# Performance work log

Hardware: AMD Instinct MI355X
Metric: run time of the kernel (lower is better)

## Reference

```python
import jax, jax.numpy as jnp
import numpy as np

D = 64        # GatedGraphConv out_channels
N_LAYERS = 5  # number of stacked convs


def setup_inputs() -> dict:
    key = jax.random.key(0)
    ks = jax.random.split(key, 16)
    N, E, G = 100000, 1600000, 64
    s = 0.1
    inp = {
        'conv_weight': jax.random.normal(ks[0], (N_LAYERS, D, D), jnp.float32) * s,
        'gru_w_ih':    jax.random.normal(ks[1], (N_LAYERS, 3 * D, D), jnp.float32) * s,
        'gru_w_hh':    jax.random.normal(ks[2], (N_LAYERS, 3 * D, D), jnp.float32) * s,
        'gru_b_ih':    jax.random.normal(ks[3], (N_LAYERS, 3 * D), jnp.float32) * s,
        'gru_b_hh':    jax.random.normal(ks[4], (N_LAYERS, 3 * D), jnp.float32) * s,
        'fc1_w': jax.random.normal(ks[5], (32, D), jnp.float32) * s,
        'fc1_b': jax.random.normal(ks[6], (32,), jnp.float32) * s,
        'fc2_w': jax.random.normal(ks[7], (16, 32), jnp.float32) * s,
        'fc2_b': jax.random.normal(ks[8], (16,), jnp.float32) * s,
        'fc3_w': jax.random.normal(ks[9], (1, 16), jnp.float32) * s,
        'fc3_b': jax.random.normal(ks[10], (1,), jnp.float32) * s,
        'edge_index': jax.random.randint(ks[11], (2, E), 0, N, jnp.int64 if jax.config.jax_enable_x64 else jnp.int32),
        'batch': jnp.sort(jax.random.randint(ks[12], (N,), 0, G, jnp.int32)),
        'num_nodes': N,
        'num_graphs': G,
    }
    return inp


def _gru_cell(m, h, w_ih, w_hh, b_ih, b_hh):
    # torch.nn.GRUCell math; m: [N,D] input, h: [N,D] hidden
    gi = m @ w_ih.T + b_ih   # [N, 3D]
    gh = h @ w_hh.T + b_hh   # [N, 3D]
    i_r, i_z, i_n = jnp.split(gi, 3, axis=1)
    h_r, h_z, h_n = jnp.split(gh, 3, axis=1)
    r = jax.nn.sigmoid(i_r + h_r)
    z = jax.nn.sigmoid(i_z + h_z)
    n = jnp.tanh(i_n + r * h_n)
    return (1.0 - z) * n + z * h


def reference(conv_weight, gru_w_ih, gru_w_hh, gru_b_ih, gru_b_hh,
              fc1_w, fc1_b, fc2_w, fc2_b, fc3_w, fc3_b,
              edge_index, batch, num_nodes, num_graphs):
    src, dst = edge_index[0], edge_index[1]  # source_to_target flow
    # initial node features: zeros [N,8] zero-padded to D by GatedGraphConv
    x0 = jnp.zeros((num_nodes, D), jnp.float32)

    def step(x, params):
        w, wih, whh, bih, bhh = params
        m = x @ w                                        # [N, D]
        agg = jax.ops.segment_sum(m[src], dst, num_segments=num_nodes)  # scatter-add
        return _gru_cell(agg, x, wih, whh, bih, bhh), None

    x, _ = jax.lax.scan(step, x0,
                        (conv_weight, gru_w_ih, gru_w_hh, gru_b_ih, gru_b_hh))

    # scatter_add pooling over batch -> [num_graphs, D]
    g = jax.ops.segment_sum(x, batch, num_segments=num_graphs)
    h = jax.nn.elu(g @ fc1_w.T + fc1_b)
    h = jax.nn.elu(h @ fc2_w.T + fc2_b)
    return h @ fc3_w.T + fc3_b  # [num_graphs, 1]
```

## Files before the change

### kernel.cpp

```cpp
#include <hip/hip_runtime.h>
#include <math.h>

typedef _Float16 f16x2 __attribute__((ext_vector_type(2)));
typedef _Float16 f16x4 __attribute__((ext_vector_type(4)));
typedef _Float16 f16x8 __attribute__((ext_vector_type(8)));
typedef float f32x4 __attribute__((ext_vector_type(4)));

#define CBITS 10
#define FCHUNK 4096
#define MATSZ 13056
#define SEGSZ 2176
#define TABN 512
__device__ __forceinline__ int woff(int row) { return 64 * row + 8 * (row >> 1); }

__device__ __forceinline__ float sigmoidf_(float v) {
  return 1.0f / (1.0f + __expf(-v));
}
__device__ __forceinline__ float tanhf_(float v) {
  v = fminf(fmaxf(v, -15.f), 15.f);
  float e = __expf(2.f * v);
  return (e - 1.f) / (e + 1.f);
}
__device__ __forceinline__ float eluf_(float v) { return v > 0.f ? v : (__expf(v) - 1.f); }

__global__ __launch_bounds__(256) void hist_kernel(const int* __restrict__ dst,
                                                   int* __restrict__ bh, int E) {
  __shared__ int h[128];
  const int t = threadIdx.x;
  if (t < 128) h[t] = 0;
  __syncthreads();
  const int e0 = blockIdx.x * FCHUNK;
  int cnt = E - e0;
  if (cnt > FCHUNK) cnt = FCHUNK;
  for (int i = t; i < cnt; i += 256) atomicAdd(&h[dst[e0 + i] >> CBITS], 1);
  __syncthreads();
  if (t < 128) bh[blockIdx.x * 128 + t] = h[t];
}

__global__ __launch_bounds__(64) void chunkscan_kernel(const int* __restrict__ bh,
                                                       int* __restrict__ cbase,
                                                       int* __restrict__ tot, int nfb) {
  const int b = blockIdx.x;
  const int lane = threadIdx.x;
  int carry = 0;
  for (int base = 0; base < nfb; base += 64) {
    int kk = base + lane;
    int v = (kk < nfb) ? bh[kk * 128 + b] : 0;
    int s = v;
#pragma unroll
    for (int o = 1; o < 64; o <<= 1) {
      int u = __shfl_up(s, o);
      if (lane >= o) s += u;
    }
    if (kk < nfb) cbase[kk * 128 + b] = carry + s - v;
    carry += __shfl(s, 63);
  }
  if (lane == 0) tot[b] = carry;
}

__global__ __launch_bounds__(256) void bucket_fill_kernel(const int* __restrict__ src,
                                                          const int* __restrict__ dst,
                                                          const int* __restrict__ bh,
                                                          const int* __restrict__ cbase,
                                                          const int* __restrict__ tot,
                                                          unsigned* __restrict__ pairs,
                                                          int E) {
  __shared__ uint2 staged[FCHUNK];
  __shared__ int h[128], lbase[128], gbase[128], lcur[128], cs[128];
  const int t = threadIdx.x;
  const int k = blockIdx.x;
  int vtot = 0;
  if (t < 128) {
    vtot = tot[t];
    cs[t] = vtot;
  }
  __syncthreads();
  for (int o = 1; o < 128; o <<= 1) {
    int a = (t < 128 && t >= o) ? cs[t - o] : 0;
    __syncthreads();
    if (t < 128) cs[t] += a;
    __syncthreads();
  }
  if (t < 128) {
    int bucketbase = cs[t] - vtot;
    gbase[t] = bucketbase + cbase[k * 128 + t];
    int myh = bh[k * 128 + t];
    h[t] = myh;
    lcur[t] = myh;
  }
  __syncthreads();
  for (int o = 1; o < 128; o <<= 1) {
    int a = (t < 128 && t >= o) ? lcur[t - o] : 0;
    __syncthreads();
    if (t < 128) lcur[t] += a;
    __syncthreads();
  }
  if (t < 128) {
    int ex = lcur[t] - h[t];
    lbase[t] = ex;
    lcur[t] = ex;
  }
  __syncthreads();
  const int e0 = k * FCHUNK;
  int cnt = E - e0;
  if (cnt > FCHUNK) cnt = FCHUNK;
  for (int i = t; i < cnt; i += 256) {
    int d = dst[e0 + i];
    int b = d >> CBITS;
    int p = atomicAdd(&lcur[b], 1);
    staged[p] = make_uint2((unsigned)src[e0 + i], (unsigned)d);
  }
  __syncthreads();
  for (int i = t; i < cnt; i += 256) {
    uint2 pr = staged[i];
    int b = (int)(pr.y >> CBITS);
    pairs[gbase[b] + (i - lbase[b])] = (pr.x << CBITS) | (pr.y & ((1u << CBITS) - 1));
  }
}

__global__ __launch_bounds__(256) void csr_build_kernel(const unsigned* __restrict__ pairs,
                                                        const int* __restrict__ tot,
                                                        int* __restrict__ offs,
                                                        int* __restrict__ srcs,
                                                        unsigned short* __restrict__ deg16,
                                                        int N, int E) {
  const int b = blockIdx.x, t = threadIdx.x;
  const int nbase = b << CBITS;
  __shared__ int deg[1024];
  __shared__ int ssc[256];
  __shared__ int cs[128];
  if (t < 128) cs[t] = tot[t];
  __syncthreads();
  for (int o = 1; o < 128; o <<= 1) {
    int a = (t < 128 && t >= o) ? cs[t - o] : 0;
    __syncthreads();
    if (t < 128) cs[t] += a;
    __syncthreads();
  }
  const int beg = (b > 0) ? cs[b - 1] : 0;
  const int end = cs[b];
  __syncthreads();
  for (int i = t; i < 1024; i += 256) deg[i] = 0;
  __syncthreads();
  for (int e = beg + t; e < end; e += 256) atomicAdd(&deg[pairs[e] & 1023], 1);
  __syncthreads();
  int d0 = deg[4 * t], d1 = deg[4 * t + 1], d2 = deg[4 * t + 2], d3 = deg[4 * t + 3];
  int s = d0 + d1 + d2 + d3;
  ssc[t] = s;
  __syncthreads();
  for (int o = 1; o < 256; o <<= 1) {
    int a = (t >= o) ? ssc[t - o] : 0;
    __syncthreads();
    ssc[t] += a;
    __syncthreads();
  }
  int base = beg + ssc[t] - s;
  int c0 = base, c1 = c0 + d0, c2 = c1 + d1, c3 = c2 + d2;
  if (nbase + 4 * t + 0 < N) { offs[nbase + 4 * t + 0] = c0; deg16[nbase + 4 * t + 0] = (unsigned short)d0; }
  if (nbase + 4 * t + 1 < N) { offs[nbase + 4 * t + 1] = c1; deg16[nbase + 4 * t + 1] = (unsigned short)d1; }
  if (nbase + 4 * t + 2 < N) { offs[nbase + 4 * t + 2] = c2; deg16[nbase + 4 * t + 2] = (unsigned short)d2; }
  if (nbase + 4 * t + 3 < N) { offs[nbase + 4 * t + 3] = c3; deg16[nbase + 4 * t + 3] = (unsigned short)d3; }
  deg[4 * t] = c0; deg[4 * t + 1] = c1; deg[4 * t + 2] = c2; deg[4 * t + 3] = c3;
  if (b == 0 && t == 0) offs[N] = E;
  if (b == 0 && t < 64) srcs[E + t] = 0;
  __syncthreads();
  for (int e = beg + t; e < end; e += 256) {
    unsigned p = pairs[e];
    int pos = atomicAdd(&deg[p & 1023], 1);
    srcs[pos] = (int)(p >> CBITS);
  }
}

__global__ __launch_bounds__(256) void wprep_kernel(const float* __restrict__ conv_w,
                                                    const float* __restrict__ w_ih,
                                                    const float* __restrict__ whh,
                                                    const float* __restrict__ b_ih,
                                                    const float* __restrict__ b_hh,
                                                    _Float16* __restrict__ wcS,
                                                    _Float16* __restrict__ whhS,
                                                    _Float16* __restrict__ tab,
                                                    float* __restrict__ gbuf, int gn) {
  __shared__ float sWt[64 * 68];
  __shared__ float sI[48 * 64];
  __shared__ float sh1[64], st[64], su[192], scons[256];
  const int t = threadIdx.x;
  if (blockIdx.x < 12) {
    const int l = 2 + (blockIdx.x >> 2);
    const int j0 = (blockIdx.x & 3) * 48;
    const float* W = conv_w + (size_t)l * 4096;
    const float* wi = w_ih + (size_t)l * 12288;
    _Float16* out = wcS + (size_t)l * MATSZ;
    for (int i = t; i < 4096; i += 256) sWt[(i & 63) * 68 + (i >> 6)] = W[i];
    for (int i = t; i < 3072; i += 256) sI[i] = wi[j0 * 64 + i];
    __syncthreads();
#pragma unroll
    for (int r = 0; r < 3; ++r) {
      int u = t + 256 * r;
      int j = u >> 4, cg = (u & 15) * 4;
      float4 a = {0.f, 0.f, 0.f, 0.f};
      for (int k = 0; k < 64; ++k) {
        float4 w = *(const float4*)(sWt + k * 68 + cg);
        float s = sI[j * 64 + k];
        a.x += w.x * s; a.y += w.y * s; a.z += w.z * s; a.w += w.w * s;
      }
      int row = j0 + j;
      f16x4 hv;
      hv[0] = (_Float16)a.x; hv[1] = (_Float16)a.y;
      hv[2] = (_Float16)a.z; hv[3] = (_Float16)a.w;
      *(f16x4*)(out + woff(row) + cg) = hv;
    }
  } else if (blockIdx.x < 48) {
    int idx = (blockIdx.x - 12) * 256 + t;
    if (idx >= 9216) return;
    int l = 2 + idx / 3072, rem = idx % 3072;
    int r = rem >> 4, c4 = (rem & 15) * 4;
    float4 v = *(const float4*)(whh + (size_t)l * 12288 + r * 64 + c4);
    f16x4 hv;
    hv[0] = (_Float16)v.x; hv[1] = (_Float16)v.y;
    hv[2] = (_Float16)v.z; hv[3] = (_Float16)v.w;
    *(f16x4*)(whhS + (size_t)l * MATSZ + woff(r) + c4) = hv;
  } else {
    for (int i = t; i < gn; i += 256) gbuf[i] = 0.f;
    if (t < 64) {
      float r = sigmoidf_(b_ih[t] + b_hh[t]);
      float z = sigmoidf_(b_ih[64 + t] + b_hh[64 + t]);
      float n = tanhf_(b_ih[128 + t] + r * b_hh[128 + t]);
      sh1[t] = (1.f - z) * n;
    }
    __syncthreads();
    if (t < 64) {
      const float* W1 = conv_w + 4096;
      float a = 0.f;
      for (int c = 0; c < 64; ++c) a += sh1[c] * W1[c * 64 + t];
      st[t] = a;
    }
    __syncthreads();
    if (t < 192) {
      const float* wih1 = w_ih + 12288;
      const float* whh1 = whh + 12288;
      float uacc = 0.f, sg = 0.f;
      for (int k = 0; k < 64; ++k) {
        uacc += wih1[t * 64 + k] * st[k];
        sg += whh1[t * 64 + k] * sh1[k];
      }
      su[t] = uacc;
      const float* bi1 = b_ih + 192;
      const float* bh1 = b_hh + 192;
      if (t < 128) {
        scons[t] = sg + bi1[t] + bh1[t];
      } else {
        scons[t] = bi1[t];
        scons[t + 64] = sg + bh1[t];
      }
    }
    __syncthreads();
    for (int idx = t; idx < TABN * 64; idx += 256) {
      int dgi = idx >> 6, j = idx & 63;
      float dg = (float)dgi;
      float r = sigmoidf_(dg * su[j] + scons[j]);
      float z = sigmoidf_(dg * su[64 + j] + scons[64 + j]);
      float n = tanhf_(dg * su[128 + j] + scons[128 + j] + r * scons[192 + j]);
      tab[idx] = (_Float16)(n + z * (sh1[j] - n));
    }
  }
}

__global__ __launch_bounds__(256) void agg2_kernel(const _Float16* __restrict__ tab,
                                                   const unsigned short* __restrict__ deg16,
                                                   const int* __restrict__ offs,
                                                   const int* __restrict__ srcs,
                                                   _Float16* __restrict__ aggh, int N) {
  int wave = threadIdx.x >> 6, lane = threadIdx.x & 63;
  int v = blockIdx.x * 4 + wave;
  if (v >= N) return;
  const int beg = offs[v], end = offs[v + 1];
  const int deg = end - beg;
  const int og = lane >> 3;
  const int lp = lane & 7;
  f16x8 acc = {};
  for (int base = 0; base < deg; base += 64) {
    const int cnt = min(64, deg - base);
    const int cnt8 = (cnt + 7) & ~7;
    int sidx = 0;
    if (lane < cnt8) sidx = srcs[beg + base + lane];
    int s0 = __shfl(sidx, og);
    int d0 = min((int)deg16[s0], TABN - 1);
    f16x8 cur = *(const f16x8*)(tab + d0 * 64 + lp * 8);
    int e = 0;
    for (; e + 8 < cnt; e += 8) {
      int sn = __shfl(sidx, e + 8 + og);
      int dn = min((int)deg16[sn], TABN - 1);
      f16x8 nxt = *(const f16x8*)(tab + dn * 64 + lp * 8);
      acc += cur;
      cur = nxt;
    }
    if (e + og < cnt) acc += cur;
  }
#pragma unroll
  for (int off = 8; off < 64; off <<= 1) {
    union { f16x8 h; int i[4]; } a, b;
    a.h = acc;
#pragma unroll
    for (int w = 0; w < 4; ++w) b.i[w] = __shfl_xor(a.i[w], off);
    acc += b.h;
  }
  if (og == 0) *(f16x8*)(aggh + (size_t)v * 64 + lp * 8) = acc;
}

__global__ __launch_bounds__(256) void agg_kernel(const _Float16* __restrict__ xh,
                                                  const int* __restrict__ offs,
                                                  const int* __restrict__ srcs,
                                                  _Float16* __restrict__ aggh, int N) {
  int wave = threadIdx.x >> 6, lane = threadIdx.x & 63;
  int v = blockIdx.x * 4 + wave;
  if (v >= N) return;
  const int beg = offs[v], end = offs[v + 1];
  const int deg = end - beg;
  const int og = lane >> 3;
  const int lp = lane & 7;
  f16x8 acc = {};
  for (int base = 0; base < deg; base += 64) {
    const int cnt = min(64, deg - base);
    const int cnt8 = (cnt + 7) & ~7;
    int sidx = 0;
    if (lane < cnt8) sidx = srcs[beg + base + lane];
    int s0 = __shfl(sidx, og);
    f16x8 cur = *(const f16x8*)(xh + (size_t)s0 * 64 + lp * 8);
    int e = 0;
    for (; e + 8 < cnt; e += 8) {
      int sn = __shfl(sidx, e + 8 + og);
      f16x8 nxt = *(const f16x8*)(xh + (size_t)sn * 64 + lp * 8);
      acc += cur;
      cur = nxt;
    }
    if (e + og < cnt) acc += cur;
  }
#pragma unroll
  for (int off = 8; off < 64; off <<= 1) {
    union { f16x8 h; int i[4]; } a, b;
    a.h = acc;
#pragma unroll
    for (int w = 0; w < 4; ++w) b.i[w] = __shfl_xor(a.i[w], off);
    acc += b.h;
  }
  if (og == 0) *(f16x8*)(aggh + (size_t)v * 64 + lp * 8) = acc;
}

template <bool TABH>
__device__ __forceinline__ void gru_body(const _Float16* __restrict__ aggh,
                                         const _Float16* __restrict__ xh_in,
                                         const unsigned short* __restrict__ deg16,
                                         const _Float16* __restrict__ tab,
                                         _Float16* __restrict__ xh_out,
                                         const _Float16* __restrict__ wcS,
                                         const _Float16* __restrict__ whhS,
                                         const float* __restrict__ b_ih,
                                         const float* __restrict__ b_hh,
                                         int N, int tiles) {
  __shared__ _Float16 sW[2 * 3 * SEGSZ];
  const int t = threadIdx.x;
  const int half = blockIdx.x & 1;
  for (int i = t; i < 1632; i += 256) {
    int mat = (i >= 816) ? 1 : 0;
    int rem = i - mat * 816;
    int seg = rem / 272;
    int u = rem % 272;
    const _Float16* srcp = (mat ? whhS : wcS) + woff(half * 32 + seg * 64) + u * 8;
    *(f16x8*)(sW + (mat * 3 + seg) * SEGSZ + u * 8) = *(const f16x8*)srcp;
  }
  __syncthreads();
  const int wave = t >> 6, lane = t & 63;
  const int q = lane >> 4, c = lane & 15;
  float bRZ[2], bZZ[2], bIN[2], bHN[2];
#pragma unroll
  for (int p = 0; p < 2; ++p) {
    int d = (half * 2 + p) * 16 + c;
    bRZ[p] = b_ih[d] + b_hh[d];
    bZZ[p] = b_ih[64 + d] + b_hh[64 + d];
    bIN[p] = b_ih[128 + d];
    bHN[p] = b_hh[128 + d];
  }
  f16x8 idf[2];
#pragma unroll
  for (int p = 0; p < 2; ++p) {
    int tgt = p * 16 + c - q * 8;
#pragma unroll
    for (int j = 0; j < 8; ++j) idf[p][j] = (j == tgt) ? (_Float16)1.0f : (_Float16)0.0f;
  }
#pragma unroll 1
  for (int tile = blockIdx.x >> 1; tile < tiles; tile += gridDim.x >> 1) {
    const int nb0 = tile * 64 + wave * 16;
    const size_t rowbase = (size_t)(nb0 + c) * 64;
    f16x8 aA[2], aH[2];
    if (TABH) {
      int dg = min((int)deg16[nb0 + c], TABN - 1);
#pragma unroll
      for (int ks = 0; ks < 2; ++ks) {
        aA[ks] = *(const f16x8*)(aggh + rowbase + ks * 32 + q * 8);
        aH[ks] = *(const f16x8*)(tab + dg * 64 + ks * 32 + q * 8);
      }
    } else {
#pragma unroll
      for (int ks = 0; ks < 2; ++ks) {
        aA[ks] = *(const f16x8*)(aggh + rowbase + ks * 32 + q * 8);
        aH[ks] = *(const f16x8*)(xh_in + rowbase + ks * 32 + q * 8);
      }
    }
    f32x4 aR[2], aZ[2], aN[2], aHNa[2], aHO[2];
#pragma unroll
    for (int p = 0; p < 2; ++p) {
      aR[p] = (f32x4){bRZ[p], bRZ[p], bRZ[p], bRZ[p]};
      aZ[p] = (f32x4){bZZ[p], bZZ[p], bZZ[p], bZZ[p]};
      aN[p] = (f32x4){bIN[p], bIN[p], bIN[p], bIN[p]};
      aHNa[p] = (f32x4){bHN[p], bHN[p], bHN[p], bHN[p]};
      aHO[p] = (f32x4){0.f, 0.f, 0.f, 0.f};
    }
#pragma unroll
    for (int ks = 0; ks < 2; ++ks) {
      const int colo = ks * 32 + q * 8;
#pragma unroll
      for (int p = 0; p < 2; ++p) {
        const int lr = p * 16 + c;
        const int ro = 64 * lr + 8 * (lr >> 1);
        f16x8 bWr = *(const f16x8*)(sW + 0 * SEGSZ + ro + colo);
        f16x8 bWz = *(const f16x8*)(sW + 1 * SEGSZ + ro + colo);
        f16x8 bWn = *(const f16x8*)(sW + 2 * SEGSZ + ro + colo);
        f16x8 bHr = *(const f16x8*)(sW + 3 * SEGSZ + ro + colo);
        f16x8 bHz = *(const f16x8*)(sW + 4 * SEGSZ + ro + colo);
        f16x8 bHn = *(const f16x8*)(sW + 5 * SEGSZ + ro + colo);
        aR[p] = __builtin_amdgcn_mfma_f32_16x16x32_f16(aA[ks], bWr, aR[p], 0, 0, 0);
        aR[p] = __builtin_amdgcn_mfma_f32_16x16x32_f16(aH[ks], bHr, aR[p], 0, 0, 0);
        aZ[p] = __builtin_amdgcn_mfma_f32_16x16x32_f16(aA[ks], bWz, aZ[p], 0, 0, 0);
        aZ[p] = __builtin_amdgcn_mfma_f32_16x16x32_f16(aH[ks], bHz, aZ[p], 0, 0, 0);
        aN[p] = __builtin_amdgcn_mfma_f32_16x16x32_f16(aA[ks], bWn, aN[p], 0, 0, 0);
        aHNa[p] = __builtin_amdgcn_mfma_f32_16x16x32_f16(aH[ks], bHn, aHNa[p], 0, 0, 0);
      }
    }
#pragma unroll
    for (int p = 0; p < 2; ++p)
      aHO[p] = __builtin_amdgcn_mfma_f32_16x16x32_f16(aH[half], idf[p], aHO[p], 0, 0, 0);
#pragma unroll
    for (int p = 0; p < 2; ++p) {
      int d = (half * 2 + p) * 16 + c;
#pragma unroll
      for (int r = 0; r < 4; ++r) {
        int node = nb0 + q * 4 + r;
        if (node < N) {
          float rr = sigmoidf_(aR[p][r]);
          float zz = sigmoidf_(aZ[p][r]);
          float nn = tanhf_(aN[p][r] + rr * aHNa[p][r]);
          float out = nn + zz * (aHO[p][r] - nn);
          xh_out[(size_t)node * 64 + d] = (_Float16)out;
        }
      }
    }
  }
}

__global__ __launch_bounds__(256) void gru_kernel(const _Float16* __restrict__ aggh,
                                                  const _Float16* __restrict__ xh_in,
                                                  _Float16* __restrict__ xh_out,
                                                  const _Float16* __restrict__ wcS,
                                                  const _Float16* __restrict__ whhS,
                                                  const float* __restrict__ b_ih,
                                                  const float* __restrict__ b_hh,
                                                  int N, int tiles) {
  gru_body<false>(aggh, xh_in, nullptr, nullptr, xh_out, wcS, whhS, b_ih, b_hh, N, tiles);
}

__global__ __launch_bounds__(256) void gru2_kernel(const _Float16* __restrict__ aggh,
                                                   const unsigned short* __restrict__ deg16,
                                                   const _Float16* __restrict__ tab,
                                                   _Float16* __restrict__ xh_out,
                                                   const _Float16* __restrict__ wcS,
                                                   const _Float16* __restrict__ whhS,
                                                   const float* __restrict__ b_ih,
                                                   const float* __restrict__ b_hh,
                                                   int N, int tiles) {
  gru_body<true>(aggh, nullptr, deg16, tab, xh_out, wcS, whhS, b_ih, b_hh, N, tiles);
}

__global__ __launch_bounds__(256) void pool_kernel(const _Float16* __restrict__ xh,
                                                   const int* __restrict__ batch,
                                                   float* __restrict__ g, int N) {
  int wave = threadIdx.x >> 6, lane = threadIdx.x & 63;
  int n0 = blockIdx.x * 64 + wave * 16;
  if (n0 >= N) return;
  int end = n0 + 16;
  if (end > N) end = N;
  int cur = batch[n0];
  float acc = 0.f;
  for (int n = n0; n < end; ++n) {
    int b = batch[n];
    if (b != cur) {
      atomicAdd(&g[(size_t)cur * 64 + lane], acc);
      acc = 0.f;
      cur = b;
    }
    acc += (float)xh[(size_t)n * 64 + lane];
  }
  atomicAdd(&g[(size_t)cur * 64 + lane], acc);
}

__global__ __launch_bounds__(256) void mlp_kernel(const float* __restrict__ g,
                                                  const float* __restrict__ w1,
                                                  const float* __restrict__ b1,
                                                  const float* __restrict__ w2,
                                                  const float* __restrict__ b2,
                                                  const float* __restrict__ w3,
                                                  const float* __restrict__ b3,
                                                  float* __restrict__ out, int G) {
  __shared__ float sG[64 * 64];
  __shared__ float sH1[64 * 32];
  __shared__ float sH2[64 * 16];
  int t = threadIdx.x;
  for (int i = t; i < G * 64; i += 256) sG[i] = g[i];
  __syncthreads();
  for (int o = t; o < G * 32; o += 256) {
    int gi = o >> 5, i = o & 31;
    float a = b1[i];
    for (int k = 0; k < 64; ++k) a += sG[gi * 64 + k] * w1[i * 64 + k];
    sH1[gi * 32 + i] = eluf_(a);
  }
  __syncthreads();
  for (int o = t; o < G * 16; o += 256) {
    int gi = o >> 4, i = o & 15;
    float a = b2[i];
    for (int k = 0; k < 32; ++k) a += sH1[gi * 32 + k] * w2[i * 32 + k];
    sH2[gi * 16 + i] = eluf_(a);
  }
  __syncthreads();
  for (int o = t; o < G; o += 256) {
    float a = b3[0];
    for (int k = 0; k < 16; ++k) a += sH2[o * 16 + k] * w3[k];
    out[o] = a;
  }
}

extern "C" void kernel_launch(void* const* d_in, const int* in_sizes, int n_in,
                              void* d_out, int out_size, void* d_ws, size_t ws_size,
                              hipStream_t stream) {
  const float* conv_w = (const float*)d_in[0];
  const float* w_ih = (const float*)d_in[1];
  const float* w_hh = (const float*)d_in[2];
  const float* b_ih = (const float*)d_in[3];
  const float* b_hh = (const float*)d_in[4];
  const float* fc1_w = (const float*)d_in[5];
  const float* fc1_b = (const float*)d_in[6];
  const float* fc2_w = (const float*)d_in[7];
  const float* fc2_b = (const float*)d_in[8];
  const float* fc3_w = (const float*)d_in[9];
  const float* fc3_b = (const float*)d_in[10];
  const int* ei = (const int*)d_in[11];
  const int* batch = (const int*)d_in[12];
  const int N = in_sizes[12];
  const int E = in_sizes[11] / 2;
  const int G = out_size;
  const int* src = ei;
  const int* dst = ei + E;
  const int nfb = (E + FCHUNK - 1) / FCHUNK;
  const int nbk = (N + 1023) >> CBITS;
  const int tiles = (N + 63) / 64;
  const int Npad = tiles * 64;

  char* ws = (char*)d_ws;
  size_t off = 0;
  auto alloc = [&](size_t bytes) -> void* {
    void* p = ws + off;
    off += (bytes + 255) & ~(size_t)255;
    return p;
  };
  _Float16* xhA = (_Float16*)alloc((size_t)Npad * 64 * 2);
  _Float16* xhB = (_Float16*)alloc((size_t)Npad * 64 * 2);
  _Float16* aggh = (_Float16*)alloc((size_t)Npad * 64 * 2);
  _Float16* wcS = (_Float16*)alloc((size_t)5 * MATSZ * 2);
  _Float16* whhS = (_Float16*)alloc((size_t)5 * MATSZ * 2);
  _Float16* h2tab = (_Float16*)alloc((size_t)TABN * 64 * 2);
  float* gbuf = (float*)alloc((size_t)G * 64 * 4);
  int* offs = (int*)alloc((size_t)(N + 1) * 4);
  int* srcs = (int*)alloc((size_t)(E + 64) * 4);
  unsigned short* deg16 = (unsigned short*)alloc((size_t)Npad * 2);
  unsigned* pairs = (unsigned*)alloc((size_t)E * 4);
  int* bh = (int*)alloc((size_t)nfb * 128 * 4);
  int* cbase = (int*)alloc((size_t)nfb * 128 * 4);
  int* tot = (int*)alloc(128 * 4);

  hist_kernel<<<nfb, 256, 0, stream>>>(dst, bh, E);
  chunkscan_kernel<<<128, 64, 0, stream>>>(bh, cbase, tot, nfb);
  bucket_fill_kernel<<<nfb, 256, 0, stream>>>(src, dst, bh, cbase, tot, pairs, E);
  csr_build_kernel<<<nbk, 256, 0, stream>>>(pairs, tot, offs, srcs, deg16, N, E);

  wprep_kernel<<<49, 256, 0, stream>>>(conv_w, w_ih, w_hh, b_ih, b_hh, wcS, whhS,
                                       h2tab, gbuf, G * 64);

  agg2_kernel<<<(N + 3) / 4, 256, 0, stream>>>(h2tab, deg16, offs, srcs, aggh, N);
  gru2_kernel<<<768, 256, 0, stream>>>(aggh, deg16, h2tab, xhA, wcS + 2 * MATSZ,
                                       whhS + 2 * MATSZ, b_ih + 2 * 192, b_hh + 2 * 192,
                                       N, tiles);
  _Float16* cur = xhA;
  _Float16* nxt = xhB;
  for (int l = 3; l < 5; ++l) {
    agg_kernel<<<(N + 3) / 4, 256, 0, stream>>>(cur, offs, srcs, aggh, N);
    gru_kernel<<<768, 256, 0, stream>>>(aggh, cur, nxt, wcS + (size_t)l * MATSZ,
                                        whhS + (size_t)l * MATSZ, b_ih + (size_t)l * 192,
                                        b_hh + (size_t)l * 192, N, tiles);
    _Float16* tmp = cur; cur = nxt; nxt = tmp;
  }

  pool_kernel<<<(N + 63) / 64, 256, 0, stream>>>(cur, batch, gbuf, N);
  mlp_kernel<<<1, 256, 0, stream>>>(gbuf, fc1_w, fc1_b, fc2_w, fc2_b, fc3_w, fc3_b,
                                    (float*)d_out, G);
}
```

Before: 390.3 us.

## Fuse neighbor aggregation, GRU update and pooling into per-layer kernels

Replaces the separate aggregation and GRU kernels with one templated kernel per layer. Each kernel gathers neighbor features, runs the MFMA GRU matmuls and applies the gate math in one pass, so the fp16 aggregate buffer is never written to or read back from global memory. The last layer accumulates the pooling sum directly into gbuf with atomics, which removes the separate pool kernel. The histogram kernel and weight-prep kernel are also merged into a single launch. The cost is a heavier kernel with more register and LDS pressure, and it launches one block per 64-node tile instead of a persistent grid of 768.

```diff
diff --git a/kernel.cpp b/kernel.cpp
--- a/kernel.cpp
+++ b/kernel.cpp
@@ -9,7 +9,7 @@
 #define CBITS 10
 #define FCHUNK 4096
 #define MATSZ 13056
-#define SEGSZ 2176
+#define GATESZ 4352
 #define TABN 512
 __device__ __forceinline__ int woff(int row) { return 64 * row + 8 * (row >> 1); }
 
@@ -23,170 +23,37 @@
 }
 __device__ __forceinline__ float eluf_(float v) { return v > 0.f ? v : (__expf(v) - 1.f); }
 
-__global__ __launch_bounds__(256) void hist_kernel(const int* __restrict__ dst,
-                                                   int* __restrict__ bh, int E) {
-  __shared__ int h[128];
-  const int t = threadIdx.x;
-  if (t < 128) h[t] = 0;
-  __syncthreads();
-  const int e0 = blockIdx.x * FCHUNK;
-  int cnt = E - e0;
-  if (cnt > FCHUNK) cnt = FCHUNK;
-  for (int i = t; i < cnt; i += 256) atomicAdd(&h[dst[e0 + i] >> CBITS], 1);
-  __syncthreads();
-  if (t < 128) bh[blockIdx.x * 128 + t] = h[t];
-}
-
-__global__ __launch_bounds__(64) void chunkscan_kernel(const int* __restrict__ bh,
-                                                       int* __restrict__ cbase,
-                                                       int* __restrict__ tot, int nfb) {
-  const int b = blockIdx.x;
-  const int lane = threadIdx.x;
-  int carry = 0;
-  for (int base = 0; base < nfb; base += 64) {
-    int kk = base + lane;
-    int v = (kk < nfb) ? bh[kk * 128 + b] : 0;
-    int s = v;
-#pragma unroll
-    for (int o = 1; o < 64; o <<= 1) {
-      int u = __shfl_up(s, o);
-      if (lane >= o) s += u;
-    }
-    if (kk < nfb) cbase[kk * 128 + b] = carry + s - v;
-    carry += __shfl(s, 63);
-  }
-  if (lane == 0) tot[b] = carry;
-}
-
-__global__ __launch_bounds__(256) void bucket_fill_kernel(const int* __restrict__ src,
-                                                          const int* __restrict__ dst,
-                                                          const int* __restrict__ bh,
-                                                          const int* __restrict__ cbase,
-                                                          const int* __restrict__ tot,
-                                                          unsigned* __restrict__ pairs,
-                                                          int E) {
-  __shared__ uint2 staged[FCHUNK];
-  __shared__ int h[128], lbase[128], gbase[128], lcur[128], cs[128];
-  const int t = threadIdx.x;
-  const int k = blockIdx.x;
-  int vtot = 0;
-  if (t < 128) {
-    vtot = tot[t];
-    cs[t] = vtot;
-  }
-  __syncthreads();
-  for (int o = 1; o < 128; o <<= 1) {
-    int a = (t < 128 && t >= o) ? cs[t - o] : 0;
-    __syncthreads();
-    if (t < 128) cs[t] += a;
-    __syncthreads();
-  }
-  if (t < 128) {
-    int bucketbase = cs[t] - vtot;
-    gbase[t] = bucketbase + cbase[k * 128 + t];
-    int myh = bh[k * 128 + t];
-    h[t] = myh;
-    lcur[t] = myh;
-  }
-  __syncthreads();
-  for (int o = 1; o < 128; o <<= 1) {
-    int a = (t < 128 && t >= o) ? lcur[t - o] : 0;
-    __syncthreads();
-    if (t < 128) lcur[t] += a;
-    __syncthreads();
-  }
-  if (t < 128) {
-    int ex = lcur[t] - h[t];
-    lbase[t] = ex;
-    lcur[t] = ex;
-  }
-  __syncthreads();
-  const int e0 = k * FCHUNK;
-  int cnt = E - e0;
-  if (cnt > FCHUNK) cnt = FCHUNK;
-  for (int i = t; i < cnt; i += 256) {
-    int d = dst[e0 + i];
-    int b = d >> CBITS;
-    int p = atomicAdd(&lcur[b], 1);
-    staged[p] = make_uint2((unsigned)src[e0 + i], (unsigned)d);
-  }
-  __syncthreads();
-  for (int i = t; i < cnt; i += 256) {
-    uint2 pr = staged[i];
-    int b = (int)(pr.y >> CBITS);
-    pairs[gbase[b] + (i - lbase[b])] = (pr.x << CBITS) | (pr.y & ((1u << CBITS) - 1));
-  }
-}
-
-__global__ __launch_bounds__(256) void csr_build_kernel(const unsigned* __restrict__ pairs,
-                                                        const int* __restrict__ tot,
-                                                        int* __restrict__ offs,
-                                                        int* __restrict__ srcs,
-                                                        unsigned short* __restrict__ deg16,
-                                                        int N, int E) {
-  const int b = blockIdx.x, t = threadIdx.x;
-  const int nbase = b << CBITS;
-  __shared__ int deg[1024];
-  __shared__ int ssc[256];
-  __shared__ int cs[128];
-  if (t < 128) cs[t] = tot[t];
-  __syncthreads();
-  for (int o = 1; o < 128; o <<= 1) {
-    int a = (t < 128 && t >= o) ? cs[t - o] : 0;
-    __syncthreads();
-    if (t < 128) cs[t] += a;
-    __syncthreads();
-  }
-  const int beg = (b > 0) ? cs[b - 1] : 0;
-  const int end = cs[b];
-  __syncthreads();
-  for (int i = t; i < 1024; i += 256) deg[i] = 0;
-  __syncthreads();
-  for (int e = beg + t; e < end; e += 256) atomicAdd(&deg[pairs[e] & 1023], 1);
-  __syncthreads();
-  int d0 = deg[4 * t], d1 = deg[4 * t + 1], d2 = deg[4 * t + 2], d3 = deg[4 * t + 3];
-  int s = d0 + d1 + d2 + d3;
-  ssc[t] = s;
-  __syncthreads();
-  for (int o = 1; o < 256; o <<= 1) {
-    int a = (t >= o) ? ssc[t - o] : 0;
-    __syncthreads();
-    ssc[t] += a;
-    __syncthreads();
-  }
-  int base = beg + ssc[t] - s;
-  int c0 = base, c1 = c0 + d0, c2 = c1 + d1, c3 = c2 + d2;
-  if (nbase + 4 * t + 0 < N) { offs[nbase + 4 * t + 0] = c0; deg16[nbase + 4 * t + 0] = (unsigned short)d0; }
-  if (nbase + 4 * t + 1 < N) { offs[nbase + 4 * t + 1] = c1; deg16[nbase + 4 * t + 1] = (unsigned short)d1; }
-  if (nbase + 4 * t + 2 < N) { offs[nbase + 4 * t + 2] = c2; deg16[nbase + 4 * t + 2] = (unsigned short)d2; }
-  if (nbase + 4 * t + 3 < N) { offs[nbase + 4 * t + 3] = c3; deg16[nbase + 4 * t + 3] = (unsigned short)d3; }
-  deg[4 * t] = c0; deg[4 * t + 1] = c1; deg[4 * t + 2] = c2; deg[4 * t + 3] = c3;
-  if (b == 0 && t == 0) offs[N] = E;
-  if (b == 0 && t < 64) srcs[E + t] = 0;
-  __syncthreads();
-  for (int e = beg + t; e < end; e += 256) {
-    unsigned p = pairs[e];
-    int pos = atomicAdd(&deg[p & 1023], 1);
-    srcs[pos] = (int)(p >> CBITS);
-  }
-}
-
-__global__ __launch_bounds__(256) void wprep_kernel(const float* __restrict__ conv_w,
-                                                    const float* __restrict__ w_ih,
-                                                    const float* __restrict__ whh,
-                                                    const float* __restrict__ b_ih,
-                                                    const float* __restrict__ b_hh,
-                                                    _Float16* __restrict__ wcS,
-                                                    _Float16* __restrict__ whhS,
-                                                    _Float16* __restrict__ tab,
-                                                    float* __restrict__ gbuf, int gn) {
+__global__ __launch_bounds__(256) void histwprep_kernel(const int* __restrict__ dst,
+                                                        int* __restrict__ bh, int E, int nfb,
+                                                        const float* __restrict__ conv_w,
+                                                        const float* __restrict__ w_ih,
+                                                        const float* __restrict__ whh,
+                                                        const float* __restrict__ b_ih,
+                                                        const float* __restrict__ b_hh,
+                                                        _Float16* __restrict__ wcS,
+                                                        _Float16* __restrict__ whhS,
+                                                        _Float16* __restrict__ tab,
+                                                        float* __restrict__ gbuf, int gn) {
   __shared__ float sWt[64 * 68];
   __shared__ float sI[48 * 64];
   __shared__ float sh1[64], st[64], su[192], scons[256];
+  __shared__ int h[128];
   const int t = threadIdx.x;
-  if (blockIdx.x < 12) {
-    const int l = 2 + (blockIdx.x >> 2);
-    const int j0 = (blockIdx.x & 3) * 48;
+  if (blockIdx.x < nfb) {
+    if (t < 128) h[t] = 0;
+    __syncthreads();
+    const int e0 = blockIdx.x * FCHUNK;
+    int cnt = E - e0;
+    if (cnt > FCHUNK) cnt = FCHUNK;
+    for (int i = t; i < cnt; i += 256) atomicAdd(&h[dst[e0 + i] >> CBITS], 1);
+    __syncthreads();
+    if (t < 128) bh[blockIdx.x * 128 + t] = h[t];
+    return;
+  }
+  const int bid = blockIdx.x - nfb;
+  if (bid < 12) {
+    const int l = 2 + (bid >> 2);
+    const int j0 = (bid & 3) * 48;
     const float* W = conv_w + (size_t)l * 4096;
     const float* wi = w_ih + (size_t)l * 12288;
     _Float16* out = wcS + (size_t)l * MATSZ;
@@ -209,8 +76,8 @@
       hv[2] = (_Float16)a.z; hv[3] = (_Float16)a.w;
       *(f16x4*)(out + woff(row) + cg) = hv;
     }
-  } else if (blockIdx.x < 48) {
-    int idx = (blockIdx.x - 12) * 256 + t;
+  } else if (bid < 48) {
+    int idx = (bid - 12) * 256 + t;
     if (idx >= 9216) return;
     int l = 2 + idx / 3072, rem = idx % 3072;
     int r = rem >> 4, c4 = (rem & 15) * 4;
@@ -265,241 +132,311 @@
   }
 }
 
-__global__ __launch_bounds__(256) void agg2_kernel(const _Float16* __restrict__ tab,
+__global__ __launch_bounds__(64) void chunkscan_kernel(const int* __restrict__ bh,
+                                                       int* __restrict__ cbase,
+                                                       int* __restrict__ tot, int nfb) {
+  const int b = blockIdx.x;
+  const int lane = threadIdx.x;
+  int carry = 0;
+  for (int base = 0; base < nfb; base += 64) {
+    int kk = base + lane;
+    int v = (kk < nfb) ? bh[kk * 128 + b] : 0;
+    int s = v;
+#pragma unroll
+    for (int o = 1; o < 64; o <<= 1) {
+      int u = __shfl_up(s, o);
+      if (lane >= o) s += u;
+    }
+    if (kk < nfb) cbase[kk * 128 + b] = carry + s - v;
+    carry += __shfl(s, 63);
+  }
+  if (lane == 0) tot[b] = carry;
+}
+
+__global__ __launch_bounds__(256) void bucket_fill_kernel(const int* __restrict__ src,
+                                                          const int* __restrict__ dst,
+                                                          const int* __restrict__ bh,
+                                                          const int* __restrict__ cbase,
+                                                          const int* __restrict__ tot,
+                                                          unsigned* __restrict__ pairs,
+                                                          int E) {
+  __shared__ uint2 staged[FCHUNK];
+  __shared__ int h[128], lbase[128], gbase[128], lcur[128], cs[128];
+  const int t = threadIdx.x;
+  const int k = blockIdx.x;
+  int vtot = 0;
+  if (t < 128) {
+    vtot = tot[t];
+    cs[t] = vtot;
+  }
+  __syncthreads();
+  for (int o = 1; o < 128; o <<= 1) {
+    int a = (t < 128 && t >= o) ? cs[t - o] : 0;
+    __syncthreads();
+    if (t < 128) cs[t] += a;
+    __syncthreads();
+  }
+  if (t < 128) {
+    int bucketbase = cs[t] - vtot;
+    gbase[t] = bucketbase + cbase[k * 128 + t];
+    int myh = bh[k * 128 + t];
+    h[t] = myh;
+    lcur[t] = myh;
+  }
+  __syncthreads();
+  for (int o = 1; o < 128; o <<= 1) {
+    int a = (t < 128 && t >= o) ? lcur[t - o] : 0;
+    __syncthreads();
+    if (t < 128) lcur[t] += a;
+    __syncthreads();
+  }
+  if (t < 128) {
+    int ex = lcur[t] - h[t];
+    lbase[t] = ex;
+    lcur[t] = ex;
+  }
+  __syncthreads();
+  const int e0 = k * FCHUNK;
+  int cnt = E - e0;
+  if (cnt > FCHUNK) cnt = FCHUNK;
+  for (int i = t; i < cnt; i += 256) {
+    int d = dst[e0 + i];
+    int b = d >> CBITS;
+    int p = atomicAdd(&lcur[b], 1);
+    staged[p] = make_uint2((unsigned)src[e0 + i], (unsigned)d);
+  }
+  __syncthreads();
+  for (int i = t; i < cnt; i += 256) {
+    uint2 pr = staged[i];
+    int b = (int)(pr.y >> CBITS);
+    pairs[gbase[b] + (i - lbase[b])] = (pr.x << CBITS) | (pr.y & ((1u << CBITS) - 1));
+  }
+}
+
+__global__ __launch_bounds__(256) void csr_build_kernel(const unsigned* __restrict__ pairs,
+                                                        const int* __restrict__ tot,
+                                                        int* __restrict__ offs,
+                                                        int* __restrict__ srcs,
+                                                        unsigned short* __restrict__ deg16,
+                                                        int N, int E) {
+  const int b = blockIdx.x, t = threadIdx.x;
+  const int nbase = b << CBITS;
+  __shared__ int deg[1024];
+  __shared__ int ssc[256];
+  __shared__ int cs[128];
+  if (t < 128) cs[t] = tot[t];
+  __syncthreads();
+  for (int o = 1; o < 128; o <<= 1) {
+    int a = (t < 128 && t >= o) ? cs[t - o] : 0;
+    __syncthreads();
+    if (t < 128) cs[t] += a;
+    __syncthreads();
+  }
+  const int beg = (b > 0) ? cs[b - 1] : 0;
+  const int end = cs[b];
+  __syncthreads();
+  for (int i = t; i < 1024; i += 256) deg[i] = 0;
+  __syncthreads();
+  for (int e = beg + t; e < end; e += 256) atomicAdd(&deg[pairs[e] & 1023], 1);
+  __syncthreads();
+  int d0 = deg[4 * t], d1 = deg[4 * t + 1], d2 = deg[4 * t + 2], d3 = deg[4 * t + 3];
+  int s = d0 + d1 + d2 + d3;
+  ssc[t] = s;
+  __syncthreads();
+  for (int o = 1; o < 256; o <<= 1) {
+    int a = (t >= o) ? ssc[t - o] : 0;
+    __syncthreads();
+    ssc[t] += a;
+    __syncthreads();
+  }
+  int base = beg + ssc[t] - s;
+  int c0 = base, c1 = c0 + d0, c2 = c1 + d1, c3 = c2 + d2;
+  if (nbase + 4 * t + 0 < N) { offs[nbase + 4 * t + 0] = c0; deg16[nbase + 4 * t + 0] = (unsigned short)d0; }
+  if (nbase + 4 * t + 1 < N) { offs[nbase + 4 * t + 1] = c1; deg16[nbase + 4 * t + 1] = (unsigned short)d1; }
+  if (nbase + 4 * t + 2 < N) { offs[nbase + 4 * t + 2] = c2; deg16[nbase + 4 * t + 2] = (unsigned short)d2; }
+  if (nbase + 4 * t + 3 < N) { offs[nbase + 4 * t + 3] = c3; deg16[nbase + 4 * t + 3] = (unsigned short)d3; }
+  deg[4 * t] = c0; deg[4 * t + 1] = c1; deg[4 * t + 2] = c2; deg[4 * t + 3] = c3;
+  if (b == 0 && t == 0) offs[N] = E;
+  if (b == 0 && t < 64) srcs[E + t] = 0;
+  __syncthreads();
+  for (int e = beg + t; e < end; e += 256) {
+    unsigned p = pairs[e];
+    int pos = atomicAdd(&deg[p & 1023], 1);
+    srcs[pos] = (int)(p >> CBITS);
+  }
+}
+
+template <int LAYER>
+__global__ __launch_bounds__(256) void fgru_kernel(const _Float16* __restrict__ xh_in,
                                                    const unsigned short* __restrict__ deg16,
+                                                   const _Float16* __restrict__ tab,
                                                    const int* __restrict__ offs,
                                                    const int* __restrict__ srcs,
-                                                   _Float16* __restrict__ aggh, int N) {
-  int wave = threadIdx.x >> 6, lane = threadIdx.x & 63;
-  int v = blockIdx.x * 4 + wave;
-  if (v >= N) return;
-  const int beg = offs[v], end = offs[v + 1];
-  const int deg = end - beg;
-  const int og = lane >> 3;
-  const int lp = lane & 7;
-  f16x8 acc = {};
-  for (int base = 0; base < deg; base += 64) {
-    const int cnt = min(64, deg - base);
-    const int cnt8 = (cnt + 7) & ~7;
-    int sidx = 0;
-    if (lane < cnt8) sidx = srcs[beg + base + lane];
-    int s0 = __shfl(sidx, og);
-    int d0 = min((int)deg16[s0], TABN - 1);
-    f16x8 cur = *(const f16x8*)(tab + d0 * 64 + lp * 8);
-    int e = 0;
-    for (; e + 8 < cnt; e += 8) {
-      int sn = __shfl(sidx, e + 8 + og);
-      int dn = min((int)deg16[sn], TABN - 1);
-      f16x8 nxt = *(const f16x8*)(tab + dn * 64 + lp * 8);
-      acc += cur;
-      cur = nxt;
-    }
-    if (e + og < cnt) acc += cur;
-  }
-#pragma unroll
-  for (int off = 8; off < 64; off <<= 1) {
-    union { f16x8 h; int i[4]; } a, b;
-    a.h = acc;
-#pragma unroll
-    for (int w = 0; w < 4; ++w) b.i[w] = __shfl_xor(a.i[w], off);
-    acc += b.h;
-  }
-  if (og == 0) *(f16x8*)(aggh + (size_t)v * 64 + lp * 8) = acc;
-}
-
-__global__ __launch_bounds__(256) void agg_kernel(const _Float16* __restrict__ xh,
-                                                  const int* __restrict__ offs,
-                                                  const int* __restrict__ srcs,
-                                                  _Float16* __restrict__ aggh, int N) {
-  int wave = threadIdx.x >> 6, lane = threadIdx.x & 63;
-  int v = blockIdx.x * 4 + wave;
-  if (v >= N) return;
-  const int beg = offs[v], end = offs[v + 1];
-  const int deg = end - beg;
-  const int og = lane >> 3;
-  const int lp = lane & 7;
-  f16x8 acc = {};
-  for (int base = 0; base < deg; base += 64) {
-    const int cnt = min(64, deg - base);
-    const int cnt8 = (cnt + 7) & ~7;
-    int sidx = 0;
-    if (lane < cnt8) sidx = srcs[beg + base + lane];
-    int s0 = __shfl(sidx, og);
-    f16x8 cur = *(const f16x8*)(xh + (size_t)s0 * 64 + lp * 8);
-    int e = 0;
-    for (; e + 8 < cnt; e += 8) {
-      int sn = __shfl(sidx, e + 8 + og);
-      f16x8 nxt = *(const f16x8*)(xh + (size_t)sn * 64 + lp * 8);
-      acc += cur;
-      cur = nxt;
-    }
-    if (e + og < cnt) acc += cur;
-  }
-#pragma unroll
-  for (int off = 8; off < 64; off <<= 1) {
-    union { f16x8 h; int i[4]; } a, b;
-    a.h = acc;
-#pragma unroll
-    for (int w = 0; w < 4; ++w) b.i[w] = __shfl_xor(a.i[w], off);
-    acc += b.h;
-  }
-  if (og == 0) *(f16x8*)(aggh + (size_t)v * 64 + lp * 8) = acc;
-}
-
-template <bool TABH>
-__device__ __forceinline__ void gru_body(const _Float16* __restrict__ aggh,
-                                         const _Float16* __restrict__ xh_in,
-                                         const unsigned short* __restrict__ deg16,
-                                         const _Float16* __restrict__ tab,
-                                         _Float16* __restrict__ xh_out,
-                                         const _Float16* __restrict__ wcS,
-                                         const _Float16* __restrict__ whhS,
-                                         const float* __restrict__ b_ih,
-                                         const float* __restrict__ b_hh,
-                                         int N, int tiles) {
-  __shared__ _Float16 sW[2 * 3 * SEGSZ];
+                                                   _Float16* __restrict__ xh_out,
+                                                   const int* __restrict__ batch,
+                                                   float* __restrict__ gbuf,
+                                                   const _Float16* __restrict__ wcS,
+                                                   const _Float16* __restrict__ whhS,
+                                                   const float* __restrict__ b_ih,
+                                                   const float* __restrict__ b_hh,
+                                                   int N) {
+  __shared__ _Float16 sW[2 * MATSZ];
+  __shared__ _Float16 aggT[4][16][72];
   const int t = threadIdx.x;
-  const int half = blockIdx.x & 1;
-  for (int i = t; i < 1632; i += 256) {
-    int mat = (i >= 816) ? 1 : 0;
-    int rem = i - mat * 816;
-    int seg = rem / 272;
-    int u = rem % 272;
-    const _Float16* srcp = (mat ? whhS : wcS) + woff(half * 32 + seg * 64) + u * 8;
-    *(f16x8*)(sW + (mat * 3 + seg) * SEGSZ + u * 8) = *(const f16x8*)srcp;
-  }
-  __syncthreads();
+  for (int i = t; i < 3264; i += 256) {
+    const _Float16* srcp = (i < 1632) ? (wcS + i * 8) : (whhS + (i - 1632) * 8);
+    *(f16x8*)(sW + i * 8) = *(const f16x8*)srcp;
+  }
   const int wave = t >> 6, lane = t & 63;
+  const int og = lane >> 3, lp = lane & 7;
+  const int nb0 = blockIdx.x * 64 + wave * 16;
+  for (int nn = 0; nn < 16; ++nn) {
+    const int v = nb0 + nn;
+    f16x8 acc = {};
+    if (v < N) {
+      const int beg = offs[v];
+      const int deg = offs[v + 1] - beg;
+      for (int base = 0; base < deg; base += 64) {
+        const int cnt = min(64, deg - base);
+        const int cnt8 = (cnt + 7) & ~7;
+        int sidx = 0;
+        if (lane < cnt8) sidx = srcs[beg + base + lane];
+        int s0 = __shfl(sidx, og);
+        f16x8 cur;
+        if (LAYER == 2) {
+          int d0 = min((int)deg16[s0], TABN - 1);
+          cur = *(const f16x8*)(tab + d0 * 64 + lp * 8);
+        } else {
+          cur = *(const f16x8*)(xh_in + (size_t)s0 * 64 + lp * 8);
+        }
+        int e = 0;
+        for (; e + 8 < cnt; e += 8) {
+          int sn = __shfl(sidx, e + 8 + og);
+          f16x8 nxt;
+          if (LAYER == 2) {
+            int dn = min((int)deg16[sn], TABN - 1);
+            nxt = *(const f16x8*)(tab + dn * 64 + lp * 8);
+          } else {
+            nxt = *(const f16x8*)(xh_in + (size_t)sn * 64 + lp * 8);
+          }
+          acc += cur;
+          cur = nxt;
+        }
+        if (e + og < cnt) acc += cur;
+      }
+#pragma unroll
+      for (int off = 8; off < 64; off <<= 1) {
+        union { f16x8 h; int i[4]; } a, b;
+        a.h = acc;
+#pragma unroll
+        for (int w = 0; w < 4; ++w) b.i[w] = __shfl_xor(a.i[w], off);
+        acc += b.h;
+      }
+    }
+    if (og == 0) *(f16x8*)(&aggT[wave][nn][lp * 8]) = acc;
+  }
+  __syncthreads();
   const int q = lane >> 4, c = lane & 15;
-  float bRZ[2], bZZ[2], bIN[2], bHN[2];
-#pragma unroll
-  for (int p = 0; p < 2; ++p) {
-    int d = (half * 2 + p) * 16 + c;
+  float bRZ[4], bZZ[4], bIN[4], bHN[4];
+#pragma unroll
+  for (int p = 0; p < 4; ++p) {
+    int d = p * 16 + c;
     bRZ[p] = b_ih[d] + b_hh[d];
     bZZ[p] = b_ih[64 + d] + b_hh[64 + d];
     bIN[p] = b_ih[128 + d];
     bHN[p] = b_hh[128 + d];
   }
-  f16x8 idf[2];
-#pragma unroll
-  for (int p = 0; p < 2; ++p) {
-    int tgt = p * 16 + c - q * 8;
-#pragma unroll
-    for (int j = 0; j < 8; ++j) idf[p][j] = (j == tgt) ? (_Float16)1.0f : (_Float16)0.0f;
-  }
-#pragma unroll 1
-  for (int tile = blockIdx.x >> 1; tile < tiles; tile += gridDim.x >> 1) {
-    const int nb0 = tile * 64 + wave * 16;
-    const size_t rowbase = (size_t)(nb0 + c) * 64;
-    f16x8 aA[2], aH[2];
-    if (TABH) {
+  f16x8 aA[2], aH[2];
+#pragma unroll
+  for (int ks = 0; ks < 2; ++ks) {
+    aA[ks] = *(const f16x8*)(&aggT[wave][c][ks * 32 + q * 8]);
+    if (LAYER == 2) {
       int dg = min((int)deg16[nb0 + c], TABN - 1);
-#pragma unroll
-      for (int ks = 0; ks < 2; ++ks) {
-        aA[ks] = *(const f16x8*)(aggh + rowbase + ks * 32 + q * 8);
-        aH[ks] = *(const f16x8*)(tab + dg * 64 + ks * 32 + q * 8);
-      }
+      aH[ks] = *(const f16x8*)(tab + dg * 64 + ks * 32 + q * 8);
     } else {
-#pragma unroll
-      for (int ks = 0; ks < 2; ++ks) {
-        aA[ks] = *(const f16x8*)(aggh + rowbase + ks * 32 + q * 8);
-        aH[ks] = *(const f16x8*)(xh_in + rowbase + ks * 32 + q * 8);
-      }
-    }
-    f32x4 aR[2], aZ[2], aN[2], aHNa[2], aHO[2];
-#pragma unroll
-    for (int p = 0; p < 2; ++p) {
-      aR[p] = (f32x4){bRZ[p], bRZ[p], bRZ[p], bRZ[p]};
-      aZ[p] = (f32x4){bZZ[p], bZZ[p], bZZ[p], bZZ[p]};
-      aN[p] = (f32x4){bIN[p], bIN[p], bIN[p], bIN[p]};
-      aHNa[p] = (f32x4){bHN[p], bHN[p], bHN[p], bHN[p]};
-      aHO[p] = (f32x4){0.f, 0.f, 0.f, 0.f};
-    }
-#pragma unroll
-    for (int ks = 0; ks < 2; ++ks) {
-      const int colo = ks * 32 + q * 8;
-#pragma unroll
-      for (int p = 0; p < 2; ++p) {
-        const int lr = p * 16 + c;
-        const int ro = 64 * lr + 8 * (lr >> 1);
-        f16x8 bWr = *(const f16x8*)(sW + 0 * SEGSZ + ro + colo);
-        f16x8 bWz = *(const f16x8*)(sW + 1 * SEGSZ + ro + colo);
-        f16x8 bWn = *(const f16x8*)(sW + 2 * SEGSZ + ro + colo);
-        f16x8 bHr = *(const f16x8*)(sW + 3 * SEGSZ + ro + colo);
-        f16x8 bHz = *(const f16x8*)(sW + 4 * SEGSZ + ro + colo);
-        f16x8 bHn = *(const f16x8*)(sW + 5 * SEGSZ + ro + colo);
-        aR[p] = __builtin_amdgcn_mfma_f32_16x16x32_f16(aA[ks], bWr, aR[p], 0, 0, 0);
-        aR[p] = __builtin_amdgcn_mfma_f32_16x16x32_f16(aH[ks], bHr, aR[p], 0, 0, 0);
-        aZ[p] = __builtin_amdgcn_mfma_f32_16x16x32_f16(aA[ks], bWz, aZ[p], 0, 0, 0);
-        aZ[p] = __builtin_amdgcn_mfma_f32_16x16x32_f16(aH[ks], bHz, aZ[p], 0, 0, 0);
-        aN[p] = __builtin_amdgcn_mfma_f32_16x16x32_f16(aA[ks], bWn, aN[p], 0, 0, 0);
-        aHNa[p] = __builtin_amdgcn_mfma_f32_16x16x32_f16(aH[ks], bHn, aHNa[p], 0, 0, 0);
-      }
-    }
-#pragma unroll
-    for (int p = 0; p < 2; ++p)
-      aHO[p] = __builtin_amdgcn_mfma_f32_16x16x32_f16(aH[half], idf[p], aHO[p], 0, 0, 0);
-#pragma unroll
-    for (int p = 0; p < 2; ++p) {
-      int d = (half * 2 + p) * 16 + c;
-#pragma unroll
-      for (int r = 0; r < 4; ++r) {
-        int node = nb0 + q * 4 + r;
-        if (node < N) {
-          float rr = sigmoidf_(aR[p][r]);
-          float zz = sigmoidf_(aZ[p][r]);
-          float nn = tanhf_(aN[p][r] + rr * aHNa[p][r]);
-          float out = nn + zz * (aHO[p][r] - nn);
+      aH[ks] = *(const f16x8*)(xh_in + (size_t)(nb0 + c) * 64 + ks * 32 + q * 8);
+    }
+  }
+  float hv[4][4];
+  if (LAYER == 2) {
+    int dgr[4];
+#pragma unroll
+    for (int r = 0; r < 4; ++r) dgr[r] = min((int)deg16[nb0 + q * 4 + r], TABN - 1);
+#pragma unroll
+    for (int p = 0; p < 4; ++p)
+#pragma unroll
+      for (int r = 0; r < 4; ++r) hv[p][r] = (float)tab[dgr[r] * 64 + p * 16 + c];
+  } else {
+#pragma unroll
+    for (int p = 0; p < 4; ++p)
+#pragma unroll
+      for (int r = 0; r < 4; ++r)
+        hv[p][r] = (float)xh_in[(size_t)(nb0 + q * 4 + r) * 64 + p * 16 + c];
+  }
+  f32x4 aR[4], aZ[4], aN[4], aHNa[4];
+#pragma unroll
+  for (int p = 0; p < 4; ++p) {
+    aR[p] = (f32x4){bRZ[p], bRZ[p], bRZ[p], bRZ[p]};
+    aZ[p] = (f32x4){bZZ[p], bZZ[p], bZZ[p], bZZ[p]};
+    aN[p] = (f32x4){bIN[p], bIN[p], bIN[p], bIN[p]};
+    aHNa[p] = (f32x4){bHN[p], bHN[p], bHN[p], bHN[p]};
+  }
+#pragma unroll
+  for (int ks = 0; ks < 2; ++ks) {
+    const int colo = ks * 32 + q * 8;
+#pragma unroll
+    for (int p = 0; p < 4; ++p) {
+      const int d = p * 16 + c;
+      const int ro = 64 * d + 8 * (d >> 1);
+      f16x8 bWr = *(const f16x8*)(sW + 0 * GATESZ + ro + colo);
+      f16x8 bWz = *(const f16x8*)(sW + 1 * GATESZ + ro + colo);
+      f16x8 bWn = *(const f16x8*)(sW + 2 * GATESZ + ro + colo);
+      f16x8 bHr = *(const f16x8*)(sW + MATSZ + 0 * GATESZ + ro + colo);
+      f16x8 bHz = *(const f16x8*)(sW + MATSZ + 1 * GATESZ + ro + colo);
+      f16x8 bHn = *(const f16x8*)(sW + MATSZ + 2 * GATESZ + ro + colo);
+      aR[p] = __builtin_amdgcn_mfma_f32_16x16x32_f16(aA[ks], bWr, aR[p], 0, 0, 0);
+      aR[p] = __builtin_amdgcn_mfma_f32_16x16x32_f16(aH[ks], bHr, aR[p], 0, 0, 0);
+      aZ[p] = __builtin_amdgcn_mfma_f32_16x16x32_f16(aA[ks], bWz, aZ[p], 0, 0, 0);
+      aZ[p] = __builtin_amdgcn_mfma_f32_16x16x32_f16(aH[ks], bHz, aZ[p], 0, 0, 0);
+      aN[p] = __builtin_amdgcn_mfma_f32_16x16x32_f16(aA[ks], bWn, aN[p], 0, 0, 0);
+      aHNa[p] = __builtin_amdgcn_mfma_f32_16x16x32_f16(aH[ks], bHn, aHNa[p], 0, 0, 0);
+    }
+  }
+  int b4[4];
+  if (LAYER == 4) {
+#pragma unroll
+    for (int r = 0; r < 4; ++r) {
+      int node = nb0 + q * 4 + r;
+      b4[r] = (node < N) ? batch[node] : -1;
+    }
+  }
+#pragma unroll
+  for (int p = 0; p < 4; ++p) {
+    const int d = p * 16 + c;
+    float pacc = 0.f;
+    int pg = -1;
+#pragma unroll
+    for (int r = 0; r < 4; ++r) {
+      int node = nb0 + q * 4 + r;
+      if (node < N) {
+        float rr = sigmoidf_(aR[p][r]);
+        float zz = sigmoidf_(aZ[p][r]);
+        float nn_ = tanhf_(aN[p][r] + rr * aHNa[p][r]);
+        float out = nn_ + zz * (hv[p][r] - nn_);
+        if (LAYER != 4) {
           xh_out[(size_t)node * 64 + d] = (_Float16)out;
+        } else {
+          if (b4[r] != pg) {
+            if (pg >= 0) atomicAdd(&gbuf[(size_t)pg * 64 + d], pacc);
+            pacc = 0.f;
+            pg = b4[r];
+          }
+          pacc += out;
         }
       }
     }
-  }
-}
-
-__global__ __launch_bounds__(256) void gru_kernel(const _Float16* __restrict__ aggh,
-                                                  const _Float16* __restrict__ xh_in,
-                                                  _Float16* __restrict__ xh_out,
-                                                  const _Float16* __restrict__ wcS,
-                                                  const _Float16* __restrict__ whhS,
-                                                  const float* __restrict__ b_ih,
-                                                  const float* __restrict__ b_hh,
-                                                  int N, int tiles) {
-  gru_body<false>(aggh, xh_in, nullptr, nullptr, xh_out, wcS, whhS, b_ih, b_hh, N, tiles);
-}
-
-__global__ __launch_bounds__(256) void gru2_kernel(const _Float16* __restrict__ aggh,
-                                                   const unsigned short* __restrict__ deg16,
-                                                   const _Float16* __restrict__ tab,
-                                                   _Float16* __restrict__ xh_out,
-                                                   const _Float16* __restrict__ wcS,
-                                                   const _Float16* __restrict__ whhS,
-                                                   const float* __restrict__ b_ih,
-                                                   const float* __restrict__ b_hh,
-                                                   int N, int tiles) {
-  gru_body<true>(aggh, nullptr, deg16, tab, xh_out, wcS, whhS, b_ih, b_hh, N, tiles);
-}
-
-__global__ __launch_bounds__(256) void pool_kernel(const _Float16* __restrict__ xh,
-                                                   const int* __restrict__ batch,
-                                                   float* __restrict__ g, int N) {
-  int wave = threadIdx.x >> 6, lane = threadIdx.x & 63;
-  int n0 = blockIdx.x * 64 + wave * 16;
-  if (n0 >= N) return;
-  int end = n0 + 16;
-  if (end > N) end = N;
-  int cur = batch[n0];
-  float acc = 0.f;
-  for (int n = n0; n < end; ++n) {
-    int b = batch[n];
-    if (b != cur) {
-      atomicAdd(&g[(size_t)cur * 64 + lane], acc);
-      acc = 0.f;
-      cur = b;
-    }
-    acc += (float)xh[(size_t)n * 64 + lane];
-  }
-  atomicAdd(&g[(size_t)cur * 64 + lane], acc);
+    if (LAYER == 4 && pg >= 0) atomicAdd(&gbuf[(size_t)pg * 64 + d], pacc);
+  }
 }
 
 __global__ __launch_bounds__(256) void mlp_kernel(const float* __restrict__ g,
@@ -572,7 +509,6 @@
   };
   _Float16* xhA = (_Float16*)alloc((size_t)Npad * 64 * 2);
   _Float16* xhB = (_Float16*)alloc((size_t)Npad * 64 * 2);
-  _Float16* aggh = (_Float16*)alloc((size_t)Npad * 64 * 2);
   _Float16* wcS = (_Float16*)alloc((size_t)5 * MATSZ * 2);
   _Float16* whhS = (_Float16*)alloc((size_t)5 * MATSZ * 2);
   _Float16* h2tab = (_Float16*)alloc((size_t)TABN * 64 * 2);
@@ -585,29 +521,22 @@
   int* cbase = (int*)alloc((size_t)nfb * 128 * 4);
   int* tot = (int*)alloc(128 * 4);
 
-  hist_kernel<<<nfb, 256, 0, stream>>>(dst, bh, E);
+  histwprep_kernel<<<nfb + 49, 256, 0, stream>>>(dst, bh, E, nfb, conv_w, w_ih, w_hh,
+                                                 b_ih, b_hh, wcS, whhS, h2tab, gbuf, G * 64);
   chunkscan_kernel<<<128, 64, 0, stream>>>(bh, cbase, tot, nfb);
   bucket_fill_kernel<<<nfb, 256, 0, stream>>>(src, dst, bh, cbase, tot, pairs, E);
   csr_build_kernel<<<nbk, 256, 0, stream>>>(pairs, tot, offs, srcs, deg16, N, E);
 
-  wprep_kernel<<<49, 256, 0, stream>>>(conv_w, w_ih, w_hh, b_ih, b_hh, wcS, whhS,
-                                       h2tab, gbuf, G * 64);
-
-  agg2_kernel<<<(N + 3) / 4, 256, 0, stream>>>(h2tab, deg16, offs, srcs, aggh, N);
-  gru2_kernel<<<768, 256, 0, stream>>>(aggh, deg16, h2tab, xhA, wcS + 2 * MATSZ,
-                                       whhS + 2 * MATSZ, b_ih + 2 * 192, b_hh + 2 * 192,
-                                       N, tiles);
-  _Float16* cur = xhA;
-  _Float16* nxt = xhB;
-  for (int l = 3; l < 5; ++l) {
-    agg_kernel<<<(N + 3) / 4, 256, 0, stream>>>(cur, offs, srcs, aggh, N);
-    gru_kernel<<<768, 256, 0, stream>>>(aggh, cur, nxt, wcS + (size_t)l * MATSZ,
-                                        whhS + (size_t)l * MATSZ, b_ih + (size_t)l * 192,
-                                        b_hh + (size_t)l * 192, N, tiles);
-    _Float16* tmp = cur; cur = nxt; nxt = tmp;
-  }
-
-  pool_kernel<<<(N + 63) / 64, 256, 0, stream>>>(cur, batch, gbuf, N);
+  fgru_kernel<2><<<tiles, 256, 0, stream>>>(nullptr, deg16, h2tab, offs, srcs, xhA,
+                                            nullptr, nullptr, wcS + 2 * MATSZ,
+                                            whhS + 2 * MATSZ, b_ih + 384, b_hh + 384, N);
+  fgru_kernel<3><<<tiles, 256, 0, stream>>>(xhA, nullptr, nullptr, offs, srcs, xhB,
+                                            nullptr, nullptr, wcS + 3 * MATSZ,
+                                            whhS + 3 * MATSZ, b_ih + 576, b_hh + 576, N);
+  fgru_kernel<4><<<tiles, 256, 0, stream>>>(xhB, nullptr, nullptr, offs, srcs, nullptr,
+                                            batch, gbuf, wcS + 4 * MATSZ,
+                                            whhS + 4 * MATSZ, b_ih + 768, b_hh + 768, N);
+
   mlp_kernel<<<1, 256, 0, stream>>>(gbuf, fc1_w, fc1_b, fc2_w, fc2_b, fc3_w, fc3_b,
                                     (float*)d_out, G);
 }
```

New measurement: 648.9 us. 66.3% more time.
